# Kernel tuning notes

Hardware: AMD Instinct MI355X
Metric: run time of the kernel (lower is better)

The kernel has to match this reference:

```python
import jax, jax.numpy as jnp
import numpy as np

H, I, E, K = 1024, 2816, 8, 2  # hidden, intermediate, n_experts, topk
B, S = 2, 2048


def setup_inputs() -> dict:
    key = jax.random.key(0)
    ks = jax.random.split(key, 6)
    def init(k, shape, fan_in):
        return (jax.random.normal(k, shape, jnp.float32) / np.sqrt(fan_in)).astype(jnp.float32)
    return {
        "x": jax.random.normal(ks[0], (B, S, H), jnp.float32),
        "Wgate": init(ks[1], (H, E), H),   # gating Linear weight (in,out layout)
        "bgate": jnp.zeros((E,), jnp.float32),  # gating Linear bias (nn.Linear default bias=True)
        "Wg": init(ks[2], (E, H, I), H),   # stacked gate_proj, mlp_bias=False
        "Wu": init(ks[3], (E, H, I), H),   # stacked up_proj
        "Wd": init(ks[4], (E, I, H), I),   # stacked down_proj
    }


def reference(x, Wgate, bgate, Wg, Wu, Wd):
    Bb, Ss, Hd = x.shape
    xf = x.reshape(-1, Hd)                       # [N, H] flattened tokens
    logits = xf @ Wgate + bgate                  # [N, E] gate logits
    topv, topi = jax.lax.top_k(logits, K)        # [N, K]
    N = xf.shape[0]
    # sparse combine weights: raw top-k LOGITS (no softmax), zeros elsewhere
    # (faithful to torch: scatter of logits_topk into -inf mask; -inf slots
    #  are never read since only selected experts contribute)
    combine = jnp.zeros_like(logits).at[jnp.arange(N)[:, None], topi].set(topv)  # [N, E]
    # dense grouped SwiGLU over all experts, then sparse combine
    g = jnp.einsum('nh,ehi->nei', xf, Wg)        # [N, E, I]
    u = jnp.einsum('nh,ehi->nei', xf, Wu)        # [N, E, I]
    h = jax.nn.silu(g) * u                       # [N, E, I]
    eo = jnp.einsum('nei,eih->neh', h, Wd)       # [N, E, H]
    out = jnp.einsum('neh,ne->nh', eo, combine).reshape(Bb, Ss, Hd)
    return out, logits
```

## Files before the change

### kernel.cpp

```cpp
#include <hip/hip_runtime.h>

#define HDIM 1024
#define IDIM 2816
#define NEXP 8
#define NTOK 4096
#define NROWS 8192
#define RPAD 8320
#define MAXT 71
#define MAXT64 136
#define GU_NYT 44
#define GU_TG 8
#define GU_NTG 9
#define GU_NWG (GU_NTG * GU_NYT * GU_TG)
#define DN_NWG (MAXT64 * 8)
#define TLDP 130

typedef short bf16x8 __attribute__((ext_vector_type(8)));
typedef float f32x4 __attribute__((ext_vector_type(4)));
typedef unsigned short u16x8 __attribute__((ext_vector_type(8)));

static __device__ __forceinline__ float bf2f(unsigned int u) {
    union { unsigned int i; float f; } v; v.i = u << 16; return v.f;
}
static __device__ __forceinline__ unsigned short f2bf(float f) {
    union { float f; unsigned int i; } v; v.f = f;
    return (unsigned short)((v.i + 0x7fffu + ((v.i >> 16) & 1u)) >> 16);
}

static __device__ __forceinline__ void gload16(const void* g, void* l) {
    __builtin_amdgcn_global_load_lds(
        (const __attribute__((address_space(1))) unsigned int*)g,
        (__attribute__((address_space(3))) unsigned int*)l, 16, 0, 0);
}

__global__ __launch_bounds__(256) void gating_kernel(
    const float* __restrict__ x, const float* __restrict__ Wgate,
    const float* __restrict__ bgate, float* __restrict__ logits_out,
    int* __restrict__ counts, int* __restrict__ topi, float* __restrict__ topv)
{
    int wave = (blockIdx.x << 2) + (threadIdx.x >> 6);
    int lane = threadIdx.x & 63;
    if (wave >= NTOK) return;
    const float* xr = x + (size_t)wave * HDIM;

    double acc[NEXP];
#pragma unroll
    for (int e = 0; e < NEXP; ++e) acc[e] = 0.0;
    for (int it = 0; it < HDIM / 64; ++it) {
        int h = lane + (it << 6);
        float xv = xr[h];
        const float* wr = Wgate + (size_t)h * NEXP;
#pragma unroll
        for (int e = 0; e < NEXP; ++e) acc[e] += (double)xv * (double)wr[e];
    }
#pragma unroll
    for (int e = 0; e < NEXP; ++e) {
        double v = acc[e];
        for (int off = 32; off; off >>= 1) v += __shfl_xor(v, off, 64);
        acc[e] = v + (double)bgate[e];
    }
    float lf[NEXP];
#pragma unroll
    for (int e = 0; e < NEXP; ++e) lf[e] = (float)acc[e];

    if (lane < NEXP) logits_out[(size_t)wave * NEXP + lane] = lf[lane];

    if (lane == 0) {
        int i1 = 0; float v1 = lf[0];
#pragma unroll
        for (int e = 1; e < NEXP; ++e) if (lf[e] > v1) { v1 = lf[e]; i1 = e; }
        int i2 = -1; float v2 = -3.0e38f;
#pragma unroll
        for (int e = 0; e < NEXP; ++e) {
            if (e == i1) continue;
            if (lf[e] > v2) { v2 = lf[e]; i2 = e; }
        }
        topi[wave * 2 + 0] = i1; topv[wave * 2 + 0] = v1;
        topi[wave * 2 + 1] = i2; topv[wave * 2 + 1] = v2;
        atomicAdd(&counts[i1], 1);
        atomicAdd(&counts[i2], 1);
    }
}

__global__ void offsets_kernel(const int* __restrict__ counts,
                               int* __restrict__ offs, int* __restrict__ cursor,
                               int* __restrict__ ntile, int* __restrict__ te,
                               int* __restrict__ tm0,
                               int* __restrict__ ntile64, int* __restrict__ te64,
                               int* __restrict__ tm64)
{
    if (threadIdx.x == 0 && blockIdx.x == 0) {
        int s = 0;
        for (int e = 0; e < NEXP; ++e) { offs[e] = s; cursor[e] = s; s += counts[e]; }
        offs[NEXP] = s;
        int nt = 0, nt64 = 0;
        for (int e = 0; e < NEXP; ++e) {
            int c = counts[e], base = offs[e];
            for (int mt = 0; mt * 128 < c; ++mt) { te[nt] = e; tm0[nt] = base + mt * 128; ++nt; }
            for (int mt = 0; mt * 64 < c; ++mt) { te64[nt64] = e; tm64[nt64] = base + mt * 64; ++nt64; }
        }
        *ntile = nt;
        *ntile64 = nt64;
    }
}

__global__ __launch_bounds__(256) void scatter_kernel(
    const float* __restrict__ x, const int* __restrict__ topi,
    const float* __restrict__ topv, int* __restrict__ cursor,
    float* __restrict__ row_w, int* __restrict__ pos_of,
    unsigned short* __restrict__ Xg)
{
    int p = (blockIdx.x << 2) + (threadIdx.x >> 6);
    int lane = threadIdx.x & 63;
    if (p >= NROWS) return;
    int n = p >> 1;
    int e = topi[p];
    float w = topv[p];
    int pos = 0;
    if (lane == 0) {
        pos = atomicAdd(&cursor[e], 1);
        row_w[pos] = w;
        pos_of[p] = pos;
    }
    pos = __shfl(pos, 0, 64);
    const float* xr = x + (size_t)n * HDIM;
    unsigned short* dst = Xg + (size_t)pos * HDIM;
#pragma unroll
    for (int it = 0; it < HDIM / 256; ++it) {
        int idx = (it * 64 + lane) * 4;
        float4 v = *reinterpret_cast<const float4*>(&xr[idx]);
        ushort4 o;
        o.x = f2bf(v.x); o.y = f2bf(v.y); o.z = f2bf(v.z); o.w = f2bf(v.w);
        *reinterpret_cast<ushort4*>(&dst[idx]) = o;
    }
}

__global__ __launch_bounds__(256) void transpose_gu_kernel(
    const float* __restrict__ Wg, const float* __restrict__ Wu,
    unsigned short* __restrict__ W2)
{
    __shared__ unsigned short lds[128 * TLDP];
    const int kind = blockIdx.z;
    const int e = blockIdx.y;
    const int tt = blockIdx.x;
    const int tr = tt / 22, tc = tt % 22;
    const int tid = threadIdx.x;

    const float* s0 = (kind ? Wu : Wg) + (size_t)e * HDIM * IDIM;
    {
        int r = tid >> 1, ch = (tid & 1) * 64;
        const float* sp = s0 + (size_t)(tr * 128 + r) * IDIM + tc * 128 + ch;
        unsigned short* lp = &lds[r * TLDP + ch];
#pragma unroll
        for (int q = 0; q < 8; ++q) {
            float4 a = *reinterpret_cast<const float4*>(sp + q * 8);
            float4 b = *reinterpret_cast<const float4*>(sp + q * 8 + 4);
            u16x8 o;
            o[0] = f2bf(a.x); o[1] = f2bf(a.y); o[2] = f2bf(a.z); o[3] = f2bf(a.w);
            o[4] = f2bf(b.x); o[5] = f2bf(b.y); o[6] = f2bf(b.z); o[7] = f2bf(b.w);
            *reinterpret_cast<u16x8*>(lp + q * 8) = o;
        }
    }
    __syncthreads();
    {
        const int g = tid & 15;
        unsigned short* d0 = W2 + (size_t)e * 2 * IDIM * HDIM + tr * 128 + g * 8;
#pragma unroll
        for (int cb = 0; cb < 8; ++cb) {
            int c = cb * 16 + (tid >> 4);
            u16x8 o;
#pragma unroll
            for (int jj = 0; jj < 8; ++jj) o[jj] = lds[(g * 8 + jj) * TLDP + c];
            int i = tc * 128 + c;
            int r2 = ((i >> 4) << 5) + (kind << 4) + (i & 15);
            *reinterpret_cast<u16x8*>(d0 + (size_t)r2 * HDIM) = o;
        }
    }
}

__global__ __launch_bounds__(256) void transpose_d_kernel(
    const float* __restrict__ Wd, unsigned short* __restrict__ Wdt)
{
    __shared__ unsigned short lds[128 * TLDP];
    const int e = blockIdx.y;
    const int tt = blockIdx.x;
    const int tr = tt / 8, tc = tt % 8;
    const int tid = threadIdx.x;

    const float* s0 = Wd + (size_t)e * IDIM * HDIM;
    {
        int r = tid >> 1, ch = (tid & 1) * 64;
        const float* sp = s0 + (size_t)(tr * 128 + r) * HDIM + tc * 128 + ch;
        unsigned short* lp = &lds[r * TLDP + ch];
#pragma unroll
        for (int q = 0; q < 8; ++q) {
            float4 a = *reinterpret_cast<const float4*>(sp + q * 8);
            float4 b = *reinterpret_cast<const float4*>(sp + q * 8 + 4);
            u16x8 o;
            o[0] = f2bf(a.x); o[1] = f2bf(a.y); o[2] = f2bf(a.z); o[3] = f2bf(a.w);
            o[4] = f2bf(b.x); o[5] = f2bf(b.y); o[6] = f2bf(b.z); o[7] = f2bf(b.w);
            *reinterpret_cast<u16x8*>(lp + q * 8) = o;
        }
    }
    __syncthreads();
    {
        const int g = tid & 15;
        unsigned short* d0 = Wdt + (size_t)e * HDIM * IDIM + tr * 128 + g * 8;
#pragma unroll
        for (int cb = 0; cb < 8; ++cb) {
            int c = cb * 16 + (tid >> 4);
            u16x8 o;
#pragma unroll
            for (int jj = 0; jj < 8; ++jj) o[jj] = lds[(g * 8 + jj) * TLDP + c];
            *reinterpret_cast<u16x8*>(d0 + (size_t)(tc * 128 + c) * IDIM) = o;
        }
    }
}

__global__ __launch_bounds__(256, 4) void gateup_kernel(
    const unsigned short* __restrict__ Xg,
    const unsigned short* __restrict__ W2,
    const int* __restrict__ offs,
    const int* __restrict__ ntile, const int* __restrict__ te,
    const int* __restrict__ tm0, unsigned short* __restrict__ hbuf)
{
    __shared__ unsigned short As[128 * 64];
    __shared__ unsigned short Bs[128 * 64];

    int bid = blockIdx.x;
    int xcd = bid & 7, rest = bid >> 3;
    int wg = xcd * (GU_NWG / 8) + rest;
    int tg = wg / (GU_NYT * GU_TG);
    int r2 = wg % (GU_NYT * GU_TG);
    int ny = r2 >> 3, ti = r2 & 7;
    int t = tg * GU_TG + ti;
    if (t >= *ntile) return;

    const int e = te[t];
    const int m0 = tm0[t];
    const int r1 = offs[e + 1];
    const int n0 = ny * 128;

    const unsigned short* wb = W2 + (size_t)e * 2 * IDIM * HDIM;

    const int tid = threadIdx.x;
    const int lane = tid & 63, wv = tid >> 6;
    const int wr = (wv >> 1) * 64, wc = (wv & 1) * 64;
    const int lr = lane & 15, kq16 = lane >> 4;

    const int a_row8 = tid >> 3;
    const int a_c16 = tid & 7;

    f32x4 zero = {0.f, 0.f, 0.f, 0.f};
    f32x4 acc[4][4];
#pragma unroll
    for (int m = 0; m < 4; ++m)
#pragma unroll
        for (int n = 0; n < 4; ++n) acc[m][n] = zero;

    for (int k0 = 0; k0 < HDIM; k0 += 64) {
        __syncthreads();
#pragma unroll
        for (int ch = 0; ch < 4; ++ch) {
            int row = ch * 32 + a_row8;
            int c16s = a_c16 ^ (row & 7);
            gload16(&Xg[(size_t)(m0 + row) * HDIM + k0 + c16s * 8], &As[ch * 2048 + tid * 8]);
            gload16(&wb[(size_t)(n0 + row) * HDIM + k0 + c16s * 8], &Bs[ch * 2048 + tid * 8]);
        }
        __syncthreads();

#pragma unroll
        for (int ks = 0; ks < 2; ++ks) {
            bf16x8 af[4], bf[4];
#pragma unroll
            for (int m = 0; m < 4; ++m) {
                int row = wr + m * 16 + lr;
                int sw = (ks * 4 + kq16) ^ (row & 7);
                af[m] = *reinterpret_cast<const bf16x8*>(&As[row * 64 + sw * 8]);
            }
#pragma unroll
            for (int n = 0; n < 4; ++n) {
                int row = wc + n * 16 + lr;
                int sw = (ks * 4 + kq16) ^ (row & 7);
                bf[n] = *reinterpret_cast<const bf16x8*>(&Bs[row * 64 + sw * 8]);
            }
#pragma unroll
            for (int m = 0; m < 4; ++m)
#pragma unroll
                for (int n = 0; n < 4; ++n)
                    acc[m][n] = __builtin_amdgcn_mfma_f32_16x16x32_bf16(af[m], bf[n], acc[m][n], 0, 0, 0);
        }
    }

    const int rr = (lane >> 4) * 4;
    const int iloc0 = ((wc >> 5) << 4) + lr;
    const int col0 = ny * 64 + iloc0;
#pragma unroll
    for (int m = 0; m < 4; ++m) {
#pragma unroll
        for (int j = 0; j < 4; ++j) {
            int grow = m0 + wr + m * 16 + rr + j;
            if (grow < r1) {
                unsigned short* hr = &hbuf[(size_t)grow * IDIM + col0];
                float g0 = acc[m][0][j], u0 = acc[m][1][j];
                float g1 = acc[m][2][j], u1 = acc[m][3][j];
                hr[0]  = f2bf(g0 / (1.0f + __expf(-g0)) * u0);
                hr[16] = f2bf(g1 / (1.0f + __expf(-g1)) * u1);
            }
        }
    }
}

__global__ __launch_bounds__(256, 4) void down_kernel(
    const unsigned short* __restrict__ hbuf,
    const unsigned short* __restrict__ Wdt,
    const int* __restrict__ offs,
    const int* __restrict__ ntile64, const int* __restrict__ te64,
    const int* __restrict__ tm64,
    const float* __restrict__ row_w,
    unsigned short* __restrict__ eobuf)
{
    __shared__ unsigned short As[64 * 64];
    __shared__ unsigned short Bs[128 * 64];

    int bid = blockIdx.x;
    int xcd = bid & 7, rest = bid >> 3;
    int wg = xcd * (DN_NWG / 8) + rest;
    int t = wg >> 3;
    int ny = wg & 7;
    if (t >= *ntile64) return;

    const int e = te64[t];
    const int m0 = tm64[t];
    const int r1 = offs[e + 1];
    const int n0 = ny * 128;

    const unsigned short* wd = Wdt + (size_t)e * HDIM * IDIM;

    const int tid = threadIdx.x;
    const int lane = tid & 63, wv = tid >> 6;
    const int wc = wv * 32;
    const int lr = lane & 15, kq16 = lane >> 4;

    const int a_row8 = tid >> 3;
    const int a_c16 = tid & 7;

    f32x4 zero = {0.f, 0.f, 0.f, 0.f};
    f32x4 acc[4][2];
#pragma unroll
    for (int m = 0; m < 4; ++m)
#pragma unroll
        for (int n = 0; n < 2; ++n) acc[m][n] = zero;

    for (int k0 = 0; k0 < IDIM; k0 += 64) {
        __syncthreads();
#pragma unroll
        for (int ch = 0; ch < 2; ++ch) {
            int row = ch * 32 + a_row8;
            int c16s = a_c16 ^ (row & 7);
            gload16(&hbuf[(size_t)(m0 + row) * IDIM + k0 + c16s * 8], &As[ch * 2048 + tid * 8]);
        }
#pragma unroll
        for (int ch = 0; ch < 4; ++ch) {
            int row = ch * 32 + a_row8;
            int c16s = a_c16 ^ (row & 7);
            gload16(&wd[(size_t)(n0 + row) * IDIM + k0 + c16s * 8], &Bs[ch * 2048 + tid * 8]);
        }
        __syncthreads();

#pragma unroll
        for (int ks = 0; ks < 2; ++ks) {
            bf16x8 af[4], bf[2];
#pragma unroll
            for (int m = 0; m < 4; ++m) {
                int row = m * 16 + lr;
                int sw = (ks * 4 + kq16) ^ (row & 7);
                af[m] = *reinterpret_cast<const bf16x8*>(&As[row * 64 + sw * 8]);
            }
#pragma unroll
            for (int n = 0; n < 2; ++n) {
                int row = wc + n * 16 + lr;
                int sw = (ks * 4 + kq16) ^ (row & 7);
                bf[n] = *reinterpret_cast<const bf16x8*>(&Bs[row * 64 + sw * 8]);
            }
#pragma unroll
            for (int m = 0; m < 4; ++m)
#pragma unroll
                for (int n = 0; n < 2; ++n)
                    acc[m][n] = __builtin_amdgcn_mfma_f32_16x16x32_bf16(af[m], bf[n], acc[m][n], 0, 0, 0);
        }
    }

    const int rr = (lane >> 4) * 4;
#pragma unroll
    for (int m = 0; m < 4; ++m) {
#pragma unroll
        for (int j = 0; j < 4; ++j) {
            int grow = m0 + m * 16 + rr + j;
            if (grow < r1) {
                float w = row_w[grow];
                unsigned short* er = &eobuf[(size_t)grow * HDIM + n0 + wc + lr];
#pragma unroll
                for (int n = 0; n < 2; ++n)
                    er[n * 16] = f2bf(acc[m][n][j] * w);
            }
        }
    }
}

__global__ __launch_bounds__(256) void combine_kernel(
    const unsigned short* __restrict__ eobuf, const int* __restrict__ pos_of,
    float* __restrict__ out)
{
    int t = blockIdx.x * 256 + threadIdx.x;
    int n = t >> 7;
    int c = (t & 127) << 3;
    int p0 = pos_of[n * 2 + 0];
    int p1 = pos_of[n * 2 + 1];
    uint4 a = *reinterpret_cast<const uint4*>(&eobuf[(size_t)p0 * HDIM + c]);
    uint4 b = *reinterpret_cast<const uint4*>(&eobuf[(size_t)p1 * HDIM + c]);
    float4 o0, o1;
    o0.x = bf2f(a.x & 0xffffu) + bf2f(b.x & 0xffffu);
    o0.y = bf2f(a.x >> 16)     + bf2f(b.x >> 16);
    o0.z = bf2f(a.y & 0xffffu) + bf2f(b.y & 0xffffu);
    o0.w = bf2f(a.y >> 16)     + bf2f(b.y >> 16);
    o1.x = bf2f(a.z & 0xffffu) + bf2f(b.z & 0xffffu);
    o1.y = bf2f(a.z >> 16)     + bf2f(b.z >> 16);
    o1.z = bf2f(a.w & 0xffffu) + bf2f(b.w & 0xffffu);
    o1.w = bf2f(a.w >> 16)     + bf2f(b.w >> 16);
    float* op = out + (size_t)n * HDIM + c;
    *reinterpret_cast<float4*>(op) = o0;
    *reinterpret_cast<float4*>(op + 4) = o1;
}

extern "C" void kernel_launch(void* const* d_in, const int* in_sizes, int n_in,
                              void* d_out, int out_size, void* d_ws, size_t ws_size,
                              hipStream_t stream)
{
    const float* x     = (const float*)d_in[0];
    const float* Wgate = (const float*)d_in[1];
    const float* bgate = (const float*)d_in[2];
    const float* Wg    = (const float*)d_in[3];
    const float* Wu    = (const float*)d_in[4];
    const float* Wd    = (const float*)d_in[5];
    float* out = (float*)d_out;
    float* logits = out + (size_t)NTOK * HDIM;

    char* ws = (char*)d_ws;
    unsigned short* Xg   = (unsigned short*)ws;
    unsigned short* hbuf = (unsigned short*)(ws + 17039360);
    unsigned short* W2   = (unsigned short*)(ws + 63897600);
    char* meta = ws + 156172288;
    int*   counts  = (int*)(meta);
    int*   offs    = (int*)(meta + 64);
    int*   cursor  = (int*)(meta + 128);
    int*   ntile   = (int*)(meta + 192);
    int*   ntile64 = (int*)(meta + 196);
    int*   te      = (int*)(meta + 256);
    int*   tm0     = (int*)(meta + 768);
    int*   te64    = (int*)(meta + 1280);
    int*   tm64    = (int*)(meta + 2048);
    int*   topi    = (int*)(meta + 4096);
    float* topv    = (float*)(meta + 36864);
    float* row_w   = (float*)(meta + 69632);
    int*   pos_of  = (int*)(meta + 102400);

    hipMemsetAsync(counts, 0, 32, stream);

    gating_kernel<<<NTOK / 4, 256, 0, stream>>>(x, Wgate, bgate, logits, counts, topi, topv);
    offsets_kernel<<<1, 64, 0, stream>>>(counts, offs, cursor, ntile, te, tm0,
                                         ntile64, te64, tm64);
    scatter_kernel<<<NROWS / 4, 256, 0, stream>>>(x, topi, topv, cursor, row_w, pos_of, Xg);

    transpose_gu_kernel<<<dim3(176, NEXP, 2), 256, 0, stream>>>(Wg, Wu, W2);

    gateup_kernel<<<GU_NWG, 256, 0, stream>>>(Xg, W2, offs, ntile, te, tm0, hbuf);

    transpose_d_kernel<<<dim3(176, NEXP), 256, 0, stream>>>(Wd, W2);

    down_kernel<<<DN_NWG, 256, 0, stream>>>(hbuf, W2, offs, ntile64, te64, tm64,
                                            row_w, Xg );

    combine_kernel<<<NTOK * HDIM / 8 / 256, 256, 0, stream>>>(Xg, pos_of, out);
}
```

Measured before the change: 489.4 us.

## Rewrite gate/up GEMM with 256x256 tiles, 8 waves and double-buffered LDS prefetch

The gate/up grouped GEMM moves from 128x128 tiles on 4 waves to 256x256 tiles on 8 waves, using 128KB of dynamic LDS split into two buffers. Loads for the next k-tile are issued during the MFMA phases of the current one, and s_setprio raises priority around the math. The aim is more operand reuse per byte loaded and hiding global-load latency behind compute. In exchange, larger tiles waste more rows on partially filled expert tiles, occupancy drops, and there are more barriers per k-step.

```diff
diff --git a/kernel.cpp b/kernel.cpp
--- a/kernel.cpp
+++ b/kernel.cpp
@@ -6,12 +6,10 @@
 #define NTOK 4096
 #define NROWS 8192
 #define RPAD 8320
-#define MAXT 71
 #define MAXT64 136
-#define GU_NYT 44
-#define GU_TG 8
-#define GU_NTG 9
-#define GU_NWG (GU_NTG * GU_NYT * GU_TG)
+#define MAXT256 40
+#define GU_NYT256 22
+#define GU_NWG (MAXT256 * GU_NYT256)
 #define DN_NWG (MAXT64 * 8)
 #define TLDP 130
 
@@ -84,8 +82,8 @@
 
 __global__ void offsets_kernel(const int* __restrict__ counts,
                                int* __restrict__ offs, int* __restrict__ cursor,
-                               int* __restrict__ ntile, int* __restrict__ te,
-                               int* __restrict__ tm0,
+                               int* __restrict__ ntile256, int* __restrict__ te256,
+                               int* __restrict__ tm256,
                                int* __restrict__ ntile64, int* __restrict__ te64,
                                int* __restrict__ tm64)
 {
@@ -93,13 +91,13 @@
         int s = 0;
         for (int e = 0; e < NEXP; ++e) { offs[e] = s; cursor[e] = s; s += counts[e]; }
         offs[NEXP] = s;
-        int nt = 0, nt64 = 0;
+        int nt256 = 0, nt64 = 0;
         for (int e = 0; e < NEXP; ++e) {
             int c = counts[e], base = offs[e];
-            for (int mt = 0; mt * 128 < c; ++mt) { te[nt] = e; tm0[nt] = base + mt * 128; ++nt; }
+            for (int mt = 0; mt * 256 < c; ++mt) { te256[nt256] = e; tm256[nt256] = base + mt * 256; ++nt256; }
             for (int mt = 0; mt * 64 < c; ++mt) { te64[nt64] = e; tm64[nt64] = base + mt * 64; ++nt64; }
         }
-        *ntile = nt;
+        *ntile256 = nt256;
         *ntile64 = nt64;
     }
 }
@@ -217,95 +215,128 @@
     }
 }
 
-__global__ __launch_bounds__(256, 4) void gateup_kernel(
+__global__ __launch_bounds__(512, 2) void gateup_kernel(
     const unsigned short* __restrict__ Xg,
     const unsigned short* __restrict__ W2,
     const int* __restrict__ offs,
-    const int* __restrict__ ntile, const int* __restrict__ te,
-    const int* __restrict__ tm0, unsigned short* __restrict__ hbuf)
-{
-    __shared__ unsigned short As[128 * 64];
-    __shared__ unsigned short Bs[128 * 64];
+    const int* __restrict__ ntile256, const int* __restrict__ te256,
+    const int* __restrict__ tm256, unsigned short* __restrict__ hbuf)
+{
+    extern __shared__ unsigned short lds[];
 
     int bid = blockIdx.x;
     int xcd = bid & 7, rest = bid >> 3;
     int wg = xcd * (GU_NWG / 8) + rest;
-    int tg = wg / (GU_NYT * GU_TG);
-    int r2 = wg % (GU_NYT * GU_TG);
-    int ny = r2 >> 3, ti = r2 & 7;
-    int t = tg * GU_TG + ti;
-    if (t >= *ntile) return;
-
-    const int e = te[t];
-    const int m0 = tm0[t];
+    int nyt = wg / MAXT256;
+    int t = wg % MAXT256;
+    if (t >= *ntile256) return;
+
+    const int e = te256[t];
+    const int m0 = tm256[t];
     const int r1 = offs[e + 1];
-    const int n0 = ny * 128;
+    const int nb = nyt * 256;
 
     const unsigned short* wb = W2 + (size_t)e * 2 * IDIM * HDIM;
 
     const int tid = threadIdx.x;
-    const int lane = tid & 63, wv = tid >> 6;
-    const int wr = (wv >> 1) * 64, wc = (wv & 1) * 64;
+    const int lane = tid & 63, wid = tid >> 6;
+    const int wm = wid >> 2, wn = wid & 3;
     const int lr = lane & 15, kq16 = lane >> 4;
 
-    const int a_row8 = tid >> 3;
-    const int a_c16 = tid & 7;
-
-    f32x4 zero = {0.f, 0.f, 0.f, 0.f};
-    f32x4 acc[4][4];
-#pragma unroll
-    for (int m = 0; m < 4; ++m)
-#pragma unroll
-        for (int n = 0; n < 4; ++n) acc[m][n] = zero;
-
-    for (int k0 = 0; k0 < HDIM; k0 += 64) {
-        __syncthreads();
-#pragma unroll
-        for (int ch = 0; ch < 4; ++ch) {
-            int row = ch * 32 + a_row8;
-            int c16s = a_c16 ^ (row & 7);
-            gload16(&Xg[(size_t)(m0 + row) * HDIM + k0 + c16s * 8], &As[ch * 2048 + tid * 8]);
-            gload16(&wb[(size_t)(n0 + row) * HDIM + k0 + c16s * 8], &Bs[ch * 2048 + tid * 8]);
-        }
-        __syncthreads();
-
-#pragma unroll
-        for (int ks = 0; ks < 2; ++ks) {
-            bf16x8 af[4], bf[4];
-#pragma unroll
-            for (int m = 0; m < 4; ++m) {
-                int row = wr + m * 16 + lr;
-                int sw = (ks * 4 + kq16) ^ (row & 7);
-                af[m] = *reinterpret_cast<const bf16x8*>(&As[row * 64 + sw * 8]);
-            }
-#pragma unroll
-            for (int n = 0; n < 4; ++n) {
-                int row = wc + n * 16 + lr;
-                int sw = (ks * 4 + kq16) ^ (row & 7);
-                bf[n] = *reinterpret_cast<const bf16x8*>(&Bs[row * 64 + sw * 8]);
-            }
-#pragma unroll
-            for (int m = 0; m < 4; ++m)
-#pragma unroll
-                for (int n = 0; n < 4; ++n)
-                    acc[m][n] = __builtin_amdgcn_mfma_f32_16x16x32_bf16(af[m], bf[n], acc[m][n], 0, 0, 0);
-        }
+    const int srow_ = tid >> 3;
+    const int swz = (tid & 7) ^ (srow_ & 7);
+
+    auto stA = [&](int kt1, int h, int buf) {
+#pragma unroll
+        for (int l = 0; l < 2; ++l) {
+            int ar = m0 + h * 128 + l * 64 + srow_;
+            ar = (ar > RPAD - 1) ? 8191 : ar;
+            gload16(&Xg[(size_t)ar * HDIM + kt1 * 64 + swz * 8],
+                    &lds[buf * 32768 + (h * 128 + l * 64) * 64 + tid * 8]);
+        }
+    };
+    auto stB = [&](int kt1, int h, int buf) {
+#pragma unroll
+        for (int l = 0; l < 2; ++l) {
+            int br = nb + h * 128 + l * 64 + srow_;
+            gload16(&wb[(size_t)br * HDIM + kt1 * 64 + swz * 8],
+                    &lds[buf * 32768 + 16384 + (h * 128 + l * 64) * 64 + tid * 8]);
+        }
+    };
+
+    f32x4 acc[8][4];
+#pragma unroll
+    for (int m = 0; m < 8; ++m)
+#pragma unroll
+        for (int n = 0; n < 4; ++n) acc[m][n] = {0.f, 0.f, 0.f, 0.f};
+
+    stA(0, 0, 0); stA(0, 1, 0); stB(0, 0, 0); stB(0, 1, 0);
+    asm volatile("s_waitcnt vmcnt(0)" ::: "memory");
+    __builtin_amdgcn_s_barrier();
+
+    for (int kt = 0; kt < HDIM / 64; ++kt) {
+        const int cur = kt & 1;
+        const int abase = cur * 32768;
+        const int bbase = cur * 32768 + 16384;
+        const bool pf = (kt + 1) < (HDIM / 64);
+#pragma unroll
+        for (int q = 0; q < 4; ++q) {
+            const int mq = (q & 1) * 4;
+            const int n2 = q >> 1;
+            bf16x8 a2[4][2], b2[2][2];
+#pragma unroll
+            for (int mm = 0; mm < 4; ++mm) {
+                int row = wm * 128 + (mq + mm) * 16 + lr;
+#pragma unroll
+                for (int ks = 0; ks < 2; ++ks) {
+                    int sw = (ks * 4 + kq16) ^ (row & 7);
+                    a2[mm][ks] = *reinterpret_cast<const bf16x8*>(&lds[abase + row * 64 + sw * 8]);
+                }
+            }
+#pragma unroll
+            for (int nn = 0; nn < 2; ++nn) {
+                int row = wn * 64 + (n2 * 2 + nn) * 16 + lr;
+#pragma unroll
+                for (int ks = 0; ks < 2; ++ks) {
+                    int sw = (ks * 4 + kq16) ^ (row & 7);
+                    b2[nn][ks] = *reinterpret_cast<const bf16x8*>(&lds[bbase + row * 64 + sw * 8]);
+                }
+            }
+            if (pf) {
+                if (q < 2) stA(kt + 1, q, cur ^ 1);
+                else       stB(kt + 1, q - 2, cur ^ 1);
+            }
+            __builtin_amdgcn_s_barrier();
+            __builtin_amdgcn_s_setprio(1);
+#pragma unroll
+            for (int ks = 0; ks < 2; ++ks)
+#pragma unroll
+                for (int mm = 0; mm < 4; ++mm)
+#pragma unroll
+                    for (int nn = 0; nn < 2; ++nn)
+                        acc[mq + mm][n2 * 2 + nn] = __builtin_amdgcn_mfma_f32_16x16x32_bf16(
+                            a2[mm][ks], b2[nn][ks], acc[mq + mm][n2 * 2 + nn], 0, 0, 0);
+            __builtin_amdgcn_s_setprio(0);
+            __builtin_amdgcn_s_barrier();
+        }
+        asm volatile("s_waitcnt vmcnt(0)" ::: "memory");
+        __builtin_amdgcn_s_barrier();
     }
 
     const int rr = (lane >> 4) * 4;
-    const int iloc0 = ((wc >> 5) << 4) + lr;
-    const int col0 = ny * 64 + iloc0;
-#pragma unroll
-    for (int m = 0; m < 4; ++m) {
+#pragma unroll
+    for (int m = 0; m < 8; ++m) {
 #pragma unroll
         for (int j = 0; j < 4; ++j) {
-            int grow = m0 + wr + m * 16 + rr + j;
+            int grow = m0 + wm * 128 + m * 16 + rr + j;
             if (grow < r1) {
-                unsigned short* hr = &hbuf[(size_t)grow * IDIM + col0];
-                float g0 = acc[m][0][j], u0 = acc[m][1][j];
-                float g1 = acc[m][2][j], u1 = acc[m][3][j];
-                hr[0]  = f2bf(g0 / (1.0f + __expf(-g0)) * u0);
-                hr[16] = f2bf(g1 / (1.0f + __expf(-g1)) * u1);
+#pragma unroll
+                for (int n2 = 0; n2 < 2; ++n2) {
+                    float g = acc[m][n2 * 2 + 0][j];
+                    float u = acc[m][n2 * 2 + 1][j];
+                    float s = g / (1.0f + __expf(-g));
+                    hbuf[(size_t)grow * IDIM + nyt * 128 + wn * 32 + n2 * 16 + lr] = f2bf(s * u);
+                }
             }
         }
     }
@@ -345,12 +376,11 @@
     const int a_row8 = tid >> 3;
     const int a_c16 = tid & 7;
 
-    f32x4 zero = {0.f, 0.f, 0.f, 0.f};
     f32x4 acc[4][2];
 #pragma unroll
     for (int m = 0; m < 4; ++m)
 #pragma unroll
-        for (int n = 0; n < 2; ++n) acc[m][n] = zero;
+        for (int n = 0; n < 2; ++n) acc[m][n] = {0.f, 0.f, 0.f, 0.f};
 
     for (int k0 = 0; k0 < IDIM; k0 += 64) {
         __syncthreads();
@@ -451,30 +481,33 @@
     unsigned short* hbuf = (unsigned short*)(ws + 17039360);
     unsigned short* W2   = (unsigned short*)(ws + 63897600);
     char* meta = ws + 156172288;
-    int*   counts  = (int*)(meta);
-    int*   offs    = (int*)(meta + 64);
-    int*   cursor  = (int*)(meta + 128);
-    int*   ntile   = (int*)(meta + 192);
-    int*   ntile64 = (int*)(meta + 196);
-    int*   te      = (int*)(meta + 256);
-    int*   tm0     = (int*)(meta + 768);
-    int*   te64    = (int*)(meta + 1280);
-    int*   tm64    = (int*)(meta + 2048);
-    int*   topi    = (int*)(meta + 4096);
-    float* topv    = (float*)(meta + 36864);
-    float* row_w   = (float*)(meta + 69632);
-    int*   pos_of  = (int*)(meta + 102400);
+    int*   counts   = (int*)(meta);
+    int*   offs     = (int*)(meta + 64);
+    int*   cursor   = (int*)(meta + 128);
+    int*   ntile256 = (int*)(meta + 192);
+    int*   ntile64  = (int*)(meta + 196);
+    int*   te64     = (int*)(meta + 1280);
+    int*   tm64     = (int*)(meta + 2048);
+    int*   te256    = (int*)(meta + 2816);
+    int*   tm256    = (int*)(meta + 2976);
+    int*   topi     = (int*)(meta + 4096);
+    float* topv     = (float*)(meta + 36864);
+    float* row_w    = (float*)(meta + 69632);
+    int*   pos_of   = (int*)(meta + 102400);
 
     hipMemsetAsync(counts, 0, 32, stream);
 
+    hipFuncSetAttribute((const void*)gateup_kernel,
+                        hipFuncAttributeMaxDynamicSharedMemorySize, 131072);
+
     gating_kernel<<<NTOK / 4, 256, 0, stream>>>(x, Wgate, bgate, logits, counts, topi, topv);
-    offsets_kernel<<<1, 64, 0, stream>>>(counts, offs, cursor, ntile, te, tm0,
+    offsets_kernel<<<1, 64, 0, stream>>>(counts, offs, cursor, ntile256, te256, tm256,
                                          ntile64, te64, tm64);
     scatter_kernel<<<NROWS / 4, 256, 0, stream>>>(x, topi, topv, cursor, row_w, pos_of, Xg);
 
     transpose_gu_kernel<<<dim3(176, NEXP, 2), 256, 0, stream>>>(Wg, Wu, W2);
 
-    gateup_kernel<<<GU_NWG, 256, 0, stream>>>(Xg, W2, offs, ntile, te, tm0, hbuf);
+    gateup_kernel<<<GU_NWG, 512, 131072, stream>>>(Xg, W2, offs, ntile256, te256, tm256, hbuf);
 
     transpose_d_kernel<<<dim3(176, NEXP), 256, 0, stream>>>(Wd, W2);
 
```

Result: slower. 530.8 us (+8.5%).
